# Optimization experiments

Hardware: AMD Instinct MI355X
Metric: run time of the kernel (lower is better)

The kernel has to match this reference:

```python
import jax, jax.numpy as jnp
import numpy as np

N_NODES = 19
N_T = 4096
LATENT = 512
HID = 2048
N_EDGES = 342


def setup_inputs() -> dict:
    key = jax.random.key(0)
    ks = jax.random.split(key, 16)
    s = lambda fan_in: 1.0 / np.sqrt(fan_in)
    d = {}
    d["latent_z"] = jax.random.normal(ks[0], (N_NODES, LATENT), dtype=jnp.float32)
    d["edge_idx"] = jax.random.randint(ks[1], (2, N_EDGES), 0, N_NODES, dtype=jnp.int64)
    # GIN layer 1 MLP: [LATENT -> HID -> HID]
    d["W1a"] = jax.random.uniform(ks[2], (LATENT, HID), jnp.float32, -s(LATENT), s(LATENT))
    d["b1a"] = jnp.zeros((HID,), jnp.float32)
    d["W1b"] = jax.random.uniform(ks[3], (HID, HID), jnp.float32, -s(HID), s(HID))
    d["b1b"] = jnp.zeros((HID,), jnp.float32)
    # GIN layer 2 MLP: [HID -> N_T -> N_T]
    d["W2a"] = jax.random.uniform(ks[4], (HID, N_T), jnp.float32, -s(HID), s(HID))
    d["b2a"] = jnp.zeros((N_T,), jnp.float32)
    d["W2b"] = jax.random.uniform(ks[5], (N_T, N_T), jnp.float32, -s(N_T), s(N_T))
    d["b2b"] = jnp.zeros((N_T,), jnp.float32)
    # Classifier: Linear(19*4096 -> LATENT), Linear(LATENT -> 1)
    fc_in = N_NODES * N_T
    d["Wc1"] = jax.random.uniform(ks[6], (fc_in, LATENT), jnp.float32, -s(fc_in), s(fc_in))
    d["bc1"] = jnp.zeros((LATENT,), jnp.float32)
    d["Wc2"] = jax.random.uniform(ks[7], (LATENT, 1), jnp.float32, -s(LATENT), s(LATENT))
    d["bc2"] = jnp.zeros((1,), jnp.float32)
    return d


def _gin_agg(h, edge_idx):
    # sum aggregation: message from src (row 0) to dst (row 1); eps = 0
    src, dst = edge_idx[0], edge_idx[1]
    agg = jax.ops.segment_sum(h[src], dst, num_segments=N_NODES)
    return h + agg


def reference(latent_z, edge_idx, W1a, b1a, W1b, b1b, W2a, b2a, W2b, b2b, Wc1, bc1, Wc2, bc2):
    # GINConv 1: nn((1+eps)*x + sum_j x_j), MLP = Lin->ReLU->Lin
    h = _gin_agg(latent_z, edge_idx)
    h = jax.nn.relu(h @ W1a + b1a) @ W1b + b1b
    h = jax.nn.relu(h)  # inter-layer activation (BasicGNN)
    # GINConv 2 (last layer: no trailing activation)
    h = _gin_agg(h, edge_idx)
    gin_recon_signal = jax.nn.relu(h @ W2a + b2a) @ W2b + b2b  # [19, 4096]
    flat = gin_recon_signal.reshape(N_NODES * N_T)
    dem_pred = jax.nn.sigmoid((flat @ Wc1 + bc1) @ Wc2 + bc2)  # [1]
    return (dem_pred, gin_recon_signal)
```

## Files before the change

### kernel.cpp

```cpp
#include <hip/hip_runtime.h>

#define NN 19
#define NT 4096
#define LAT 512
#define HID 2048
#define NE 342

__global__ __launch_bounds__(512) void agg1_kernel(const float* __restrict__ z,
                                                   const int* __restrict__ eidx,
                                                   float* __restrict__ h0,
                                                   float* __restrict__ Mout) {
    __shared__ int cnt[NN * NN];
    __shared__ float M[NN * NN];
    __shared__ int nzflag;
    const int t = threadIdx.x;
    if (t == 0) nzflag = 0;
    for (int i = t; i < NN * NN; i += 512) cnt[i] = 0;
    __syncthreads();
    if (t < 128 && eidx[2 * t + 1] != 0) atomicOr(&nzflag, 1);
    __syncthreads();
    const bool i64 = (nzflag == 0);
    if (t < NE) {
        const int s = i64 ? eidx[2 * t] : eidx[t];
        const int d = i64 ? eidx[2 * NE + 2 * t] : eidx[NE + t];
        atomicAdd(&cnt[d * NN + s], 1);
    }
    __syncthreads();
    for (int i = t; i < NN * NN; i += 512) {
        const float v = (float)cnt[i] + ((i / NN) == (i % NN) ? 1.f : 0.f);
        M[i] = v;
        Mout[i] = v;
    }
    __syncthreads();
    float zv[NN];
#pragma unroll
    for (int i = 0; i < NN; ++i) zv[i] = z[i * LAT + t];
#pragma unroll
    for (int d = 0; d < NN; ++d) {
        float acc = 0.f;
#pragma unroll
        for (int s = 0; s < NN; ++s) acc = fmaf(M[d * NN + s], zv[s], acc);
        h0[d * LAT + t] = acc;
    }
}

template <int BK>
__global__ __launch_bounds__(256) void gemm19p(const float* __restrict__ A,
                                               const float* __restrict__ W,
                                               float* __restrict__ part,
                                               int N) {
    __shared__ float sA[BK][20];
    const int K = gridDim.y * BK;
    const int k0 = blockIdx.y * BK;
    for (int idx = threadIdx.x; idx < NN * BK; idx += 256) {
        const int i = idx / BK, c = idx % BK;
        sA[c][i] = A[(size_t)i * K + k0 + c];
    }
    __syncthreads();

    const int col = 2 * (blockIdx.x * 256 + threadIdx.x);
    const float* __restrict__ w = W + (size_t)k0 * N + col;
    float2 acc[NN];
#pragma unroll
    for (int i = 0; i < NN; ++i) acc[i] = make_float2(0.f, 0.f);

    for (int kk = 0; kk < BK; kk += 8) {
        float2 wb[8];
#pragma unroll
        for (int u = 0; u < 8; ++u)
            wb[u] = *(const float2*)(w + (size_t)(kk + u) * N);
#pragma unroll
        for (int u = 0; u < 8; ++u) {
#pragma unroll
            for (int i = 0; i < NN; ++i) {
                const float av = sA[kk + u][i];
                acc[i].x = fmaf(av, wb[u].x, acc[i].x);
                acc[i].y = fmaf(av, wb[u].y, acc[i].y);
            }
        }
    }
    float* __restrict__ p = part + (size_t)(blockIdx.y * NN) * N + col;
#pragma unroll
    for (int i = 0; i < NN; ++i) *(float2*)(p + (size_t)i * N) = acc[i];
}

__global__ __launch_bounds__(256) void reduce_relu(const float* __restrict__ part,
                                                   const float* __restrict__ bias,
                                                   float* __restrict__ out,
                                                   int N4, int nchunk) {
    const int f = blockIdx.x * 256 + threadIdx.x;
    const int i = f / N4, n4 = f % N4;
    const float4 b = ((const float4*)bias)[n4];
    float4 s = b;
    const float4* __restrict__ p = (const float4*)part + (size_t)i * N4 + n4;
    for (int c = 0; c < nchunk; ++c) {
        const float4 v = p[(size_t)c * NN * N4];
        s.x += v.x; s.y += v.y; s.z += v.z; s.w += v.w;
    }
    s.x = s.x > 0.f ? s.x : 0.f;
    s.y = s.y > 0.f ? s.y : 0.f;
    s.z = s.z > 0.f ? s.z : 0.f;
    s.w = s.w > 0.f ? s.w : 0.f;
    ((float4*)out)[(size_t)i * N4 + n4] = s;
}

__global__ __launch_bounds__(256) void reduce_out(const float* __restrict__ part,
                                                  const float* __restrict__ bias,
                                                  float* __restrict__ out,
                                                  int N4, int nchunk) {
    const int f = blockIdx.x * 256 + threadIdx.x;
    const int i = f / N4, n4 = f % N4;
    const float4 b = ((const float4*)bias)[n4];
    float4 s = b;
    const float4* __restrict__ p = (const float4*)part + (size_t)i * N4 + n4;
    for (int c = 0; c < nchunk; ++c) {
        const float4 v = p[(size_t)c * NN * N4];
        s.x += v.x; s.y += v.y; s.z += v.z; s.w += v.w;
    }
    float* __restrict__ o = out + ((size_t)i * N4 + n4) * 4;
    o[0] = s.x; o[1] = s.y; o[2] = s.z; o[3] = s.w;
}

__global__ __launch_bounds__(256) void agg19(const float* __restrict__ h,
                                             const float* __restrict__ Mg,
                                             float* __restrict__ out,
                                             int N4) {
    __shared__ float M[NN * NN];
    const int t = threadIdx.x;
    for (int i = t; i < NN * NN; i += 256) M[i] = Mg[i];
    __syncthreads();
    const int f = blockIdx.x * 256 + t;
    const int d = f / N4, n4 = f % N4;
    float4 acc = make_float4(0.f, 0.f, 0.f, 0.f);
#pragma unroll
    for (int s = 0; s < NN; ++s) {
        const float m = M[d * NN + s];
        const float4 v = ((const float4*)h)[(size_t)s * N4 + n4];
        acc.x = fmaf(m, v.x, acc.x);
        acc.y = fmaf(m, v.y, acc.y);
        acc.z = fmaf(m, v.z, acc.z);
        acc.w = fmaf(m, v.w, acc.w);
    }
    ((float4*)out)[(size_t)d * N4 + n4] = acc;
}

__global__ __launch_bounds__(256) void cls_partial(const float* __restrict__ flat,
                                                   const float* __restrict__ Wc1,
                                                   float* __restrict__ part,
                                                   int BK) {
    __shared__ float4 comb[128];
    const int t = threadIdx.x;
    const int n4 = t & 127, kp = t >> 7;
    const int k0 = blockIdx.x * BK;
    const float4* __restrict__ w = (const float4*)Wc1 + (size_t)k0 * 128 + n4;
    const float* __restrict__ f = flat + k0;
    float4 acc = make_float4(0.f, 0.f, 0.f, 0.f);
    for (int k = kp; k < BK; k += 16) {
        float4 wb[8];
        float fv[8];
#pragma unroll
        for (int u = 0; u < 8; ++u) wb[u] = w[(size_t)(k + 2 * u) * 128];
#pragma unroll
        for (int u = 0; u < 8; ++u) fv[u] = f[k + 2 * u];
#pragma unroll
        for (int u = 0; u < 8; ++u) {
            acc.x = fmaf(fv[u], wb[u].x, acc.x);
            acc.y = fmaf(fv[u], wb[u].y, acc.y);
            acc.z = fmaf(fv[u], wb[u].z, acc.z);
            acc.w = fmaf(fv[u], wb[u].w, acc.w);
        }
    }
    if (kp) comb[n4] = acc;
    __syncthreads();
    if (!kp) {
        const float4 o = comb[n4];
        acc.x += o.x; acc.y += o.y; acc.z += o.z; acc.w += o.w;
        ((float4*)part)[(size_t)blockIdx.x * 128 + n4] = acc;
    }
}

__global__ __launch_bounds__(256) void cls_reduce(const float* __restrict__ part,
                                                  float* __restrict__ part2) {
    const int g = blockIdx.x;
    const int t = threadIdx.x;
    float2 acc = make_float2(0.f, 0.f);
#pragma unroll
    for (int c = 0; c < 16; ++c) {
        const float2 v = *(const float2*)(part + (size_t)(g * 16 + c) * LAT + 2 * t);
        acc.x += v.x;
        acc.y += v.y;
    }
    *(float2*)(part2 + (size_t)g * LAT + 2 * t) = acc;
}

__global__ __launch_bounds__(512) void cls_final(const float* __restrict__ part2,
                                                 const float* __restrict__ bc1,
                                                 const float* __restrict__ Wc2,
                                                 const float* __restrict__ bc2,
                                                 float* __restrict__ out) {
    __shared__ float red[512];
    const int t = threadIdx.x;
    float s = bc1[t];
#pragma unroll
    for (int g = 0; g < 16; ++g) s += part2[(size_t)g * LAT + t];
    red[t] = s * Wc2[t];
    __syncthreads();
    for (int off = 256; off > 0; off >>= 1) {
        if (t < off) red[t] += red[t + off];
        __syncthreads();
    }
    if (t == 0) {
        const float x = red[0] + bc2[0];
        out[0] = 1.f / (1.f + expf(-x));
    }
}

extern "C" void kernel_launch(void* const* d_in, const int* in_sizes, int n_in,
                              void* d_out, int out_size, void* d_ws, size_t ws_size,
                              hipStream_t stream) {
    const float* z   = (const float*)d_in[0];
    const int*   ei  = (const int*)d_in[1];
    const float* W1a = (const float*)d_in[2];
    const float* b1a = (const float*)d_in[3];
    const float* W1b = (const float*)d_in[4];
    const float* b1b = (const float*)d_in[5];
    const float* W2a = (const float*)d_in[6];
    const float* b2a = (const float*)d_in[7];
    const float* W2b = (const float*)d_in[8];
    const float* b2b = (const float*)d_in[9];
    const float* Wc1 = (const float*)d_in[10];
    const float* bc1 = (const float*)d_in[11];
    const float* Wc2 = (const float*)d_in[12];
    const float* bc2 = (const float*)d_in[13];
    float* out = (float*)d_out;
    float* ws  = (float*)d_ws;

    float* Mws   = ws + 0;
    float* h0    = ws + 1024;
    float* h1a   = ws + 16384;
    float* h1r   = ws + 65536;
    float* h2    = ws + 114688;
    float* t2    = ws + 163840;
    float* part  = ws + 262144;
    float* part2 = ws + 3145728;

    agg1_kernel<<<1, 512, 0, stream>>>(z, ei, h0, Mws);
    gemm19p<32><<<dim3(4, 16), 256, 0, stream>>>(h0, W1a, part, HID);
    reduce_relu<<<38, 256, 0, stream>>>(part, b1a, h1a, HID / 4, 16);
    gemm19p<64><<<dim3(4, 32), 256, 0, stream>>>(h1a, W1b, part, HID);
    reduce_relu<<<38, 256, 0, stream>>>(part, b1b, h1r, HID / 4, 32);
    agg19<<<38, 256, 0, stream>>>(h1r, Mws, h2, HID / 4);

    gemm19p<128><<<dim3(8, 16), 256, 0, stream>>>(h2, W2a, part, NT);
    reduce_relu<<<76, 256, 0, stream>>>(part, b2a, t2, NT / 4, 16);
    gemm19p<128><<<dim3(8, 32), 256, 0, stream>>>(t2, W2b, part, NT);
    reduce_out<<<76, 256, 0, stream>>>(part, b2b, out + 1, NT / 4, 32);

    cls_partial<<<256, 256, 0, stream>>>(out + 1, Wc1, part, 304);
    cls_reduce<<<16, 256, 0, stream>>>(part, part2);
    cls_final<<<1, 512, 0, stream>>>(part2, bc1, Wc2, bc2, out);
}
```

Baseline: 187.6 us.

## Fuse whole GNN pipeline into one cooperative persistent kernel with grid syncs

Replaces thirteen separate kernel launches with a single cooperative kernel of 256 blocks that walks through every stage and separates them with grid-wide syncs. Each block folds the GIN aggregation into its GEMM A-tile load, so the standalone aggregation kernels go away. GEMM tiles change to float4 columns with smaller K chunks, which gives more blocks per stage and more partial sums to reduce. The aim is to remove launch overhead and inter-kernel gaps and to raise memory parallelism in the weight-streaming GEMMs. In exchange, every grid sync leaves idle blocks waiting on the slowest one, and the partial-sum buffers become larger.

Measured after the change: 402.3 us. +114.4%, slower.

```diff
diff --git a/kernel.cpp b/kernel.cpp
--- a/kernel.cpp
+++ b/kernel.cpp
@@ -1,4 +1,7 @@
 #include <hip/hip_runtime.h>
+#include <hip/hip_cooperative_groups.h>
+
+namespace cg = cooperative_groups;
 
 #define NN 19
 #define NT 4096
@@ -6,156 +9,165 @@
 #define HID 2048
 #define NE 342
 
-__global__ __launch_bounds__(512) void agg1_kernel(const float* __restrict__ z,
-                                                   const int* __restrict__ eidx,
-                                                   float* __restrict__ h0,
-                                                   float* __restrict__ Mout) {
-    __shared__ int cnt[NN * NN];
-    __shared__ float M[NN * NN];
-    __shared__ int nzflag;
-    const int t = threadIdx.x;
-    if (t == 0) nzflag = 0;
-    for (int i = t; i < NN * NN; i += 512) cnt[i] = 0;
-    __syncthreads();
-    if (t < 128 && eidx[2 * t + 1] != 0) atomicOr(&nzflag, 1);
-    __syncthreads();
-    const bool i64 = (nzflag == 0);
-    if (t < NE) {
-        const int s = i64 ? eidx[2 * t] : eidx[t];
-        const int d = i64 ? eidx[2 * NE + 2 * t] : eidx[NE + t];
+#define LDS_F    4416
+#define SA_OFF   0
+#define SZ_OFF   2688
+#define M_OFF    4032
+#define FLAG_OFF 4400
+
+__device__ __forceinline__ void build_M(const int* __restrict__ ei, float* lds, int t) {
+    float* M = lds + M_OFF;
+    int* cnt = (int*)(lds + SZ_OFF);
+    int* flag = (int*)(lds + FLAG_OFF);
+    if (t == 0) *flag = 0;
+    for (int i = t; i < NN * NN; i += 256) cnt[i] = 0;
+    __syncthreads();
+    int f = 0;
+    for (int i = t; i < NE; i += 256) f |= ei[2 * i + 1];
+    if (f) atomicOr(flag, 1);
+    __syncthreads();
+    const bool i64 = (*flag == 0);
+    for (int i = t; i < NE; i += 256) {
+        const int s = i64 ? ei[2 * i] : ei[i];
+        const int d = i64 ? ei[2 * NE + 2 * i] : ei[NE + i];
         atomicAdd(&cnt[d * NN + s], 1);
     }
     __syncthreads();
-    for (int i = t; i < NN * NN; i += 512) {
-        const float v = (float)cnt[i] + ((i / NN) == (i % NN) ? 1.f : 0.f);
-        M[i] = v;
-        Mout[i] = v;
-    }
-    __syncthreads();
-    float zv[NN];
-#pragma unroll
-    for (int i = 0; i < NN; ++i) zv[i] = z[i * LAT + t];
-#pragma unroll
-    for (int d = 0; d < NN; ++d) {
-        float acc = 0.f;
-#pragma unroll
-        for (int s = 0; s < NN; ++s) acc = fmaf(M[d * NN + s], zv[s], acc);
-        h0[d * LAT + t] = acc;
-    }
-}
-
-template <int BK>
-__global__ __launch_bounds__(256) void gemm19p(const float* __restrict__ A,
-                                               const float* __restrict__ W,
-                                               float* __restrict__ part,
-                                               int N) {
-    __shared__ float sA[BK][20];
-    const int K = gridDim.y * BK;
-    const int k0 = blockIdx.y * BK;
-    for (int idx = threadIdx.x; idx < NN * BK; idx += 256) {
-        const int i = idx / BK, c = idx % BK;
-        sA[c][i] = A[(size_t)i * K + k0 + c];
-    }
-    __syncthreads();
-
-    const int col = 2 * (blockIdx.x * 256 + threadIdx.x);
-    const float* __restrict__ w = W + (size_t)k0 * N + col;
-    float2 acc[NN];
-#pragma unroll
-    for (int i = 0; i < NN; ++i) acc[i] = make_float2(0.f, 0.f);
-
+    for (int i = t; i < NN * NN; i += 256)
+        M[i] = (float)cnt[i] + ((i / NN) == (i % NN) ? 1.f : 0.f);
+    __syncthreads();
+}
+
+template <int BK, int N>
+__device__ __forceinline__ void gemm_inner(int t, int kc, int cb,
+                                           const float* __restrict__ W,
+                                           float* __restrict__ part,
+                                           const float* __restrict__ sA) {
+    const int k0 = kc * BK;
+    const int col = cb * 1024 + 4 * t;
+    const float4* __restrict__ w = (const float4*)(W + (size_t)k0 * N + col);
+    float4 acc[NN];
+#pragma unroll
+    for (int i = 0; i < NN; ++i) acc[i] = make_float4(0.f, 0.f, 0.f, 0.f);
+#pragma unroll 1
     for (int kk = 0; kk < BK; kk += 8) {
-        float2 wb[8];
-#pragma unroll
-        for (int u = 0; u < 8; ++u)
-            wb[u] = *(const float2*)(w + (size_t)(kk + u) * N);
+        float4 wb[8];
+#pragma unroll
+        for (int u = 0; u < 8; ++u) wb[u] = w[(size_t)(kk + u) * (N / 4)];
 #pragma unroll
         for (int u = 0; u < 8; ++u) {
 #pragma unroll
             for (int i = 0; i < NN; ++i) {
-                const float av = sA[kk + u][i];
+                const float av = sA[(kk + u) * 21 + i];
                 acc[i].x = fmaf(av, wb[u].x, acc[i].x);
                 acc[i].y = fmaf(av, wb[u].y, acc[i].y);
+                acc[i].z = fmaf(av, wb[u].z, acc[i].z);
+                acc[i].w = fmaf(av, wb[u].w, acc[i].w);
             }
         }
     }
-    float* __restrict__ p = part + (size_t)(blockIdx.y * NN) * N + col;
-#pragma unroll
-    for (int i = 0; i < NN; ++i) *(float2*)(p + (size_t)i * N) = acc[i];
-}
-
-__global__ __launch_bounds__(256) void reduce_relu(const float* __restrict__ part,
-                                                   const float* __restrict__ bias,
-                                                   float* __restrict__ out,
-                                                   int N4, int nchunk) {
-    const int f = blockIdx.x * 256 + threadIdx.x;
-    const int i = f / N4, n4 = f % N4;
-    const float4 b = ((const float4*)bias)[n4];
-    float4 s = b;
-    const float4* __restrict__ p = (const float4*)part + (size_t)i * N4 + n4;
-    for (int c = 0; c < nchunk; ++c) {
-        const float4 v = p[(size_t)c * NN * N4];
-        s.x += v.x; s.y += v.y; s.z += v.z; s.w += v.w;
-    }
-    s.x = s.x > 0.f ? s.x : 0.f;
-    s.y = s.y > 0.f ? s.y : 0.f;
-    s.z = s.z > 0.f ? s.z : 0.f;
-    s.w = s.w > 0.f ? s.w : 0.f;
-    ((float4*)out)[(size_t)i * N4 + n4] = s;
-}
-
-__global__ __launch_bounds__(256) void reduce_out(const float* __restrict__ part,
-                                                  const float* __restrict__ bias,
-                                                  float* __restrict__ out,
-                                                  int N4, int nchunk) {
-    const int f = blockIdx.x * 256 + threadIdx.x;
-    const int i = f / N4, n4 = f % N4;
-    const float4 b = ((const float4*)bias)[n4];
-    float4 s = b;
-    const float4* __restrict__ p = (const float4*)part + (size_t)i * N4 + n4;
-    for (int c = 0; c < nchunk; ++c) {
-        const float4 v = p[(size_t)c * NN * N4];
-        s.x += v.x; s.y += v.y; s.z += v.z; s.w += v.w;
-    }
-    float* __restrict__ o = out + ((size_t)i * N4 + n4) * 4;
-    o[0] = s.x; o[1] = s.y; o[2] = s.z; o[3] = s.w;
-}
-
-__global__ __launch_bounds__(256) void agg19(const float* __restrict__ h,
-                                             const float* __restrict__ Mg,
-                                             float* __restrict__ out,
-                                             int N4) {
-    __shared__ float M[NN * NN];
-    const int t = threadIdx.x;
-    for (int i = t; i < NN * NN; i += 256) M[i] = Mg[i];
-    __syncthreads();
-    const int f = blockIdx.x * 256 + t;
-    const int d = f / N4, n4 = f % N4;
-    float4 acc = make_float4(0.f, 0.f, 0.f, 0.f);
-#pragma unroll
-    for (int s = 0; s < NN; ++s) {
-        const float m = M[d * NN + s];
-        const float4 v = ((const float4*)h)[(size_t)s * N4 + n4];
-        acc.x = fmaf(m, v.x, acc.x);
-        acc.y = fmaf(m, v.y, acc.y);
-        acc.z = fmaf(m, v.z, acc.z);
-        acc.w = fmaf(m, v.w, acc.w);
-    }
-    ((float4*)out)[(size_t)d * N4 + n4] = acc;
-}
-
-__global__ __launch_bounds__(256) void cls_partial(const float* __restrict__ flat,
-                                                   const float* __restrict__ Wc1,
-                                                   float* __restrict__ part,
-                                                   int BK) {
-    __shared__ float4 comb[128];
-    const int t = threadIdx.x;
-    const int n4 = t & 127, kp = t >> 7;
-    const int k0 = blockIdx.x * BK;
-    const float4* __restrict__ w = (const float4*)Wc1 + (size_t)k0 * 128 + n4;
+    float* __restrict__ p = part + (size_t)kc * NN * N + col;
+#pragma unroll
+    for (int i = 0; i < NN; ++i) *(float4*)(p + (size_t)i * N) = acc[i];
+}
+
+template <int BK, int K, int N>
+__device__ __forceinline__ void gemm_plain(int bid, int t, const float* __restrict__ A,
+                                           const float* __restrict__ W,
+                                           float* __restrict__ part, float* lds) {
+    const int NCB = N / 1024;
+    const int kc = bid / NCB, cb = bid % NCB;
+    const int k0 = kc * BK;
+    float* sA = lds + SA_OFF;
+    for (int idx = t; idx < NN * BK; idx += 256) {
+        const int i = idx / BK, c = idx % BK;
+        sA[c * 21 + i] = A[(size_t)i * K + k0 + c];
+    }
+    __syncthreads();
+    gemm_inner<BK, N>(t, kc, cb, W, part, sA);
+    __syncthreads();
+}
+
+template <int BK, int K, int N>
+__device__ __forceinline__ void gemm_from_M(int bid, int t, const float* __restrict__ Asrc,
+                                            const float* __restrict__ W,
+                                            float* __restrict__ part, float* lds,
+                                            const int* __restrict__ ei) {
+    const int NCB = N / 1024;
+    const int kc = bid / NCB, cb = bid % NCB;
+    const int k0 = kc * BK;
+    build_M(ei, lds, t);
+    float* sA = lds + SA_OFF;
+    float* sZ = lds + SZ_OFF;
+    float* M = lds + M_OFF;
+    for (int idx = t; idx < NN * BK; idx += 256) {
+        const int s = idx / BK, c = idx % BK;
+        sZ[c * 21 + s] = Asrc[(size_t)s * K + k0 + c];
+    }
+    __syncthreads();
+    for (int idx = t; idx < NN * BK; idx += 256) {
+        const int i = idx / BK, c = idx % BK;
+        float acc = 0.f;
+#pragma unroll
+        for (int s = 0; s < NN; ++s) acc = fmaf(M[i * NN + s], sZ[c * 21 + s], acc);
+        sA[c * 21 + i] = acc;
+    }
+    __syncthreads();
+    gemm_inner<BK, N>(t, kc, cb, W, part, sA);
+    __syncthreads();
+}
+
+__device__ __forceinline__ void reduce_stage(int bid, int t, const float* __restrict__ part,
+                                             const float* __restrict__ bias,
+                                             float* __restrict__ outp,
+                                             int N4, int nchunk, bool relu) {
+    const int idx = bid * 256 + t;
+    if (idx < NN * N4) {
+        const int i = idx / N4, n4 = idx % N4;
+        float4 s = ((const float4*)bias)[n4];
+        const float4* __restrict__ p = (const float4*)part + (size_t)i * N4 + n4;
+        for (int c = 0; c < nchunk; ++c) {
+            const float4 v = p[(size_t)c * NN * N4];
+            s.x += v.x; s.y += v.y; s.z += v.z; s.w += v.w;
+        }
+        if (relu) {
+            s.x = s.x > 0.f ? s.x : 0.f;
+            s.y = s.y > 0.f ? s.y : 0.f;
+            s.z = s.z > 0.f ? s.z : 0.f;
+            s.w = s.w > 0.f ? s.w : 0.f;
+        }
+        ((float4*)outp)[(size_t)i * N4 + n4] = s;
+    }
+}
+
+__device__ __forceinline__ void reduce_out_stage(int bid, int t, const float* __restrict__ part,
+                                                 const float* __restrict__ bias,
+                                                 float* __restrict__ outp,
+                                                 int N4, int nchunk) {
+    const int idx = bid * 256 + t;
+    if (idx < NN * N4) {
+        const int i = idx / N4, n4 = idx % N4;
+        float4 s = ((const float4*)bias)[n4];
+        const float4* __restrict__ p = (const float4*)part + (size_t)i * N4 + n4;
+        for (int c = 0; c < nchunk; ++c) {
+            const float4 v = p[(size_t)c * NN * N4];
+            s.x += v.x; s.y += v.y; s.z += v.z; s.w += v.w;
+        }
+        float* __restrict__ o = outp + ((size_t)i * N4 + n4) * 4;
+        o[0] = s.x; o[1] = s.y; o[2] = s.z; o[3] = s.w;
+    }
+}
+
+__device__ __forceinline__ void cls_stage(int bid, int t, const float* __restrict__ flat,
+                                          const float* __restrict__ Wc1,
+                                          float* __restrict__ part, float* lds) {
+    const int q = t & 127, kp = t >> 7;
+    const int k0 = bid * 304;
+    const float4* __restrict__ w = (const float4*)Wc1 + (size_t)k0 * 128 + q;
     const float* __restrict__ f = flat + k0;
     float4 acc = make_float4(0.f, 0.f, 0.f, 0.f);
-    for (int k = kp; k < BK; k += 16) {
+#pragma unroll 1
+    for (int k = kp; k < 304; k += 16) {
         float4 wb[8];
         float fv[8];
 #pragma unroll
@@ -170,48 +182,81 @@
             acc.w = fmaf(fv[u], wb[u].w, acc.w);
         }
     }
-    if (kp) comb[n4] = acc;
+    float4* comb = (float4*)lds;
+    __syncthreads();
+    if (kp) comb[q] = acc;
     __syncthreads();
     if (!kp) {
-        const float4 o = comb[n4];
+        const float4 o = comb[q];
         acc.x += o.x; acc.y += o.y; acc.z += o.z; acc.w += o.w;
-        ((float4*)part)[(size_t)blockIdx.x * 128 + n4] = acc;
-    }
-}
-
-__global__ __launch_bounds__(256) void cls_reduce(const float* __restrict__ part,
-                                                  float* __restrict__ part2) {
-    const int g = blockIdx.x;
+        ((float4*)part)[(size_t)bid * 128 + q] = acc;
+    }
+}
+
+__global__ void __launch_bounds__(256, 2)
+fused_gnn(const float* __restrict__ z, const int* __restrict__ ei,
+          const float* __restrict__ W1a, const float* __restrict__ b1a,
+          const float* __restrict__ W1b, const float* __restrict__ b1b,
+          const float* __restrict__ W2a, const float* __restrict__ b2a,
+          const float* __restrict__ W2b, const float* __restrict__ b2b,
+          const float* __restrict__ Wc1, const float* __restrict__ bc1,
+          const float* __restrict__ Wc2, const float* __restrict__ bc2,
+          float* __restrict__ out, float* __restrict__ ws) {
+    cg::grid_group grid = cg::this_grid();
+    __shared__ __align__(16) float lds[LDS_F];
     const int t = threadIdx.x;
-    float2 acc = make_float2(0.f, 0.f);
-#pragma unroll
-    for (int c = 0; c < 16; ++c) {
-        const float2 v = *(const float2*)(part + (size_t)(g * 16 + c) * LAT + 2 * t);
-        acc.x += v.x;
-        acc.y += v.y;
-    }
-    *(float2*)(part2 + (size_t)g * LAT + 2 * t) = acc;
-}
-
-__global__ __launch_bounds__(512) void cls_final(const float* __restrict__ part2,
-                                                 const float* __restrict__ bc1,
-                                                 const float* __restrict__ Wc2,
-                                                 const float* __restrict__ bc2,
-                                                 float* __restrict__ out) {
-    __shared__ float red[512];
-    const int t = threadIdx.x;
-    float s = bc1[t];
-#pragma unroll
-    for (int g = 0; g < 16; ++g) s += part2[(size_t)g * LAT + t];
-    red[t] = s * Wc2[t];
-    __syncthreads();
-    for (int off = 256; off > 0; off >>= 1) {
-        if (t < off) red[t] += red[t + off];
+    const int bid = blockIdx.x;
+
+    float* h1a   = ws + 16384;
+    float* h1r   = ws + 65536;
+    float* t2    = ws + 163840;
+    float* part  = ws + 262144;
+    float* part2 = ws + 5242880;
+
+    if (bid < 32) gemm_from_M<32, LAT, HID>(bid, t, z, W1a, part, lds, ei);
+    grid.sync();
+    if (bid < 38) reduce_stage(bid, t, part, b1a, h1a, HID / 4, 16, true);
+    grid.sync();
+    if (bid < 128) gemm_plain<32, HID, HID>(bid, t, h1a, W1b, part, lds);
+    grid.sync();
+    if (bid < 38) reduce_stage(bid, t, part, b1b, h1r, HID / 4, 64, true);
+    grid.sync();
+    gemm_from_M<32, HID, NT>(bid, t, h1r, W2a, part, lds, ei);
+    grid.sync();
+    if (bid < 76) reduce_stage(bid, t, part, b2a, t2, NT / 4, 64, true);
+    grid.sync();
+    gemm_plain<64, NT, NT>(bid, t, t2, W2b, part, lds);
+    grid.sync();
+    if (bid < 76) reduce_out_stage(bid, t, part, b2b, out + 1, NT / 4, 64);
+    grid.sync();
+    cls_stage(bid, t, out + 1, Wc1, part, lds);
+    grid.sync();
+    if (bid < 16) {
+        float2 s = make_float2(0.f, 0.f);
+#pragma unroll
+        for (int c = 0; c < 16; ++c) {
+            const float2 v = *(const float2*)(part + (size_t)(bid * 16 + c) * LAT + 2 * t);
+            s.x += v.x; s.y += v.y;
+        }
+        *(float2*)(part2 + (size_t)bid * LAT + 2 * t) = s;
+    }
+    grid.sync();
+    if (bid == 0) {
+        float2 s = make_float2(bc1[2 * t], bc1[2 * t + 1]);
+#pragma unroll
+        for (int g = 0; g < 16; ++g) {
+            const float2 v = *(const float2*)(part2 + (size_t)g * LAT + 2 * t);
+            s.x += v.x; s.y += v.y;
+        }
+        float r = s.x * Wc2[2 * t] + s.y * Wc2[2 * t + 1];
+        float* red = lds;
+        red[t] = r;
         __syncthreads();
-    }
-    if (t == 0) {
-        const float x = red[0] + bc2[0];
-        out[0] = 1.f / (1.f + expf(-x));
+        for (int off = 128; off > 0; off >>= 1) {
+            if (t < off) red[t] += red[t + off];
+            __syncthreads();
+        }
+        if (t == 0) out[0] = 1.f / (1.f + expf(-(red[0] + bc2[0])));
     }
 }
 
@@ -235,28 +280,7 @@
     float* out = (float*)d_out;
     float* ws  = (float*)d_ws;
 
-    float* Mws   = ws + 0;
-    float* h0    = ws + 1024;
-    float* h1a   = ws + 16384;
-    float* h1r   = ws + 65536;
-    float* h2    = ws + 114688;
-    float* t2    = ws + 163840;
-    float* part  = ws + 262144;
-    float* part2 = ws + 3145728;
-
-    agg1_kernel<<<1, 512, 0, stream>>>(z, ei, h0, Mws);
-    gemm19p<32><<<dim3(4, 16), 256, 0, stream>>>(h0, W1a, part, HID);
-    reduce_relu<<<38, 256, 0, stream>>>(part, b1a, h1a, HID / 4, 16);
-    gemm19p<64><<<dim3(4, 32), 256, 0, stream>>>(h1a, W1b, part, HID);
-    reduce_relu<<<38, 256, 0, stream>>>(part, b1b, h1r, HID / 4, 32);
-    agg19<<<38, 256, 0, stream>>>(h1r, Mws, h2, HID / 4);
-
-    gemm19p<128><<<dim3(8, 16), 256, 0, stream>>>(h2, W2a, part, NT);
-    reduce_relu<<<76, 256, 0, stream>>>(part, b2a, t2, NT / 4, 16);
-    gemm19p<128><<<dim3(8, 32), 256, 0, stream>>>(t2, W2b, part, NT);
-    reduce_out<<<76, 256, 0, stream>>>(part, b2b, out + 1, NT / 4, 32);
-
-    cls_partial<<<256, 256, 0, stream>>>(out + 1, Wc1, part, 304);
-    cls_reduce<<<16, 256, 0, stream>>>(part, part2);
-    cls_final<<<1, 512, 0, stream>>>(part2, bc1, Wc2, bc2, out);
-}
+    void* args[] = {&z, &ei, &W1a, &b1a, &W1b, &b1b, &W2a, &b2a, &W2b, &b2b,
+                    &Wc1, &bc1, &Wc2, &bc2, &out, &ws};
+    hipLaunchCooperativeKernel((void*)fused_gnn, dim3(256), dim3(256), args, 0, stream);
+}
```
